# Kernel tuning notes

Hardware: AMD Instinct MI355X
Metric: run time of the kernel (lower is better)

Reference implementation:

```python
import jax, jax.numpy as jnp
import numpy as np

B, C, H, W = 32, 1536, 14, 14   # input is (B*4, C, H, W); joint -> (B, C, 2H, 2W)
CI = C // 2                     # non-local inter_channels
EPS = 1e-5


def conv1x1(x, w, b):
    # x: (b, cin, h, w); w: (cout, cin); b: (cout,)
    return jnp.einsum('bchw,oc->bohw', x, w) + b[None, :, None, None]


def maxpool2(x):
    b, c, h, w = x.shape
    return x.reshape(b, c, h // 2, 2, w // 2, 2).max(axis=(3, 5))


def setup_inputs():
    key = jax.random.key(0)
    ks = jax.random.split(key, 12)
    s = 0.02
    return {
        'x': jax.random.normal(ks[0], (B * 4, C, H, W), jnp.float32),
        'w_theta': jax.random.normal(ks[1], (CI, C), jnp.float32) * s,
        'b_theta': jnp.zeros((CI,), jnp.float32),
        'w_phi': jax.random.normal(ks[2], (CI, C), jnp.float32) * s,
        'b_phi': jnp.zeros((CI,), jnp.float32),
        'w_g': jax.random.normal(ks[3], (CI, C), jnp.float32) * s,
        'b_g': jnp.zeros((CI,), jnp.float32),
        'w_W': jax.random.normal(ks[4], (C, CI), jnp.float32) * s,
        'b_W': jnp.zeros((C,), jnp.float32),
        'bn_gamma': jax.random.normal(ks[5], (C,), jnp.float32) * 0.1 + 1.0,
        'bn_beta': jax.random.normal(ks[6], (C,), jnp.float32) * 0.1,
        'bn_mean': jax.random.normal(ks[7], (C,), jnp.float32) * 0.1,
        'bn_var': jnp.ones((C,), jnp.float32),
    }


def joint(x):
    # (B*4, C, H, W) -> (B, C, 2H, 2W): 4 views tiled in a 2x2 grid
    x4 = x.reshape(B, 4, C, H, W)
    top = jnp.concatenate([x4[:, 0], x4[:, 1]], axis=-1)   # (B, C, H, 2W)
    bot = jnp.concatenate([x4[:, 2], x4[:, 3]], axis=-1)
    return jnp.concatenate([top, bot], axis=-2)             # (B, C, 2H, 2W)


def reference(x, w_theta, b_theta, w_phi, b_phi, w_g, b_g, w_W, b_W,
              bn_gamma, bn_beta, bn_mean, bn_var):
    xj = joint(x)                                           # (B, C, Hj, Wj)
    b, c, hj, wj = xj.shape
    n = hj * wj                                             # 784 query positions

    theta = conv1x1(xj, w_theta, b_theta).reshape(b, CI, n)             # (B, CI, N)
    phi = maxpool2(conv1x1(xj, w_phi, b_phi)).reshape(b, CI, -1)        # (B, CI, N/4)
    g = maxpool2(conv1x1(xj, w_g, b_g)).reshape(b, CI, -1)              # (B, CI, N/4)

    f = jnp.einsum('bcn,bcm->bnm', theta, phi)              # (B, N, N/4)
    attn = jax.nn.softmax(f, axis=-1)
    y = jnp.einsum('bnm,bcm->bcn', attn, g)                 # (B, CI, N)
    y = y.reshape(b, CI, hj, wj)

    w_y = conv1x1(y, w_W, b_W)
    # BatchNorm (inference form)
    inv = jax.lax.rsqrt(bn_var + EPS)
    w_y = (w_y - bn_mean[None, :, None, None]) * (bn_gamma * inv)[None, :, None, None] \
          + bn_beta[None, :, None, None]
    return w_y + xj
```

## Files before the change

### kernel.cpp

```cpp
#include <hip/hip_runtime.h>
#include <hip/hip_bf16.h>

typedef __attribute__((ext_vector_type(8))) _Float16 f16x8;
typedef __attribute__((ext_vector_type(4))) float f32x4;
typedef __attribute__((ext_vector_type(4))) unsigned short us4;
typedef __attribute__((ext_vector_type(8))) unsigned short us8;

#define B_   32
#define C_   1536
#define CI_  768
#define N_   784
#define S_   196
#define MP_  224
#define MK_  196

__device__ __forceinline__ unsigned short f2h(float f) {
    _Float16 h = (_Float16)f;
    return __builtin_bit_cast(unsigned short, h);
}
__device__ __forceinline__ f32x4 mfma_f16(f16x8 a, f16x8 b, f32x4 c) {
    return __builtin_amdgcn_mfma_f32_16x16x32_f16(a, b, c, 0, 0, 0);
}
__device__ __forceinline__ void gl_lds16(const unsigned short* g, unsigned short* l) {
    __builtin_amdgcn_global_load_lds(
        (const __attribute__((address_space(1))) unsigned int*)g,
        (__attribute__((address_space(3))) unsigned int*)l, 16, 0, 0);
}

__device__ __forceinline__ void stage23(const unsigned short* Arow,
                                        const unsigned short* Brow,
                                        unsigned short* A_s, unsigned short* B_s,
                                        int k0, int stride,
                                        int wv, int l4r, int l4c_sw) {
    for (int c = wv; c < 23; c += 4) {
        if (c < 16) {
            gl_lds16(Arow + (size_t)(c * 16 + l4r) * stride + k0 + l4c_sw * 8,
                     A_s + c * 512);
        } else {
            int cb = c - 16;
            gl_lds16(Brow + (size_t)(cb * 16 + l4r) * stride + k0 + l4c_sw * 8,
                     B_s + cb * 512);
        }
    }
}

__device__ __forceinline__ void stage24(const unsigned short* Arow,
                                        const unsigned short* Brow,
                                        unsigned short* A_s, unsigned short* B_s,
                                        int k0, int stride,
                                        int wv, int l4r, int l4c_sw) {
    for (int c = wv; c < 24; c += 4) {
        if (c < 16) {
            gl_lds16(Arow + (size_t)(c * 16 + l4r) * stride + k0 + l4c_sw * 8,
                     A_s + c * 512);
        } else {
            int cb = c - 16;
            gl_lds16(Brow + (size_t)(cb * 16 + l4r) * stride + k0 + l4c_sw * 8,
                     B_s + cb * 512);
        }
    }
}

#define PIPE_WAIT_BARRIER()                                   \
    do {                                                      \
        asm volatile("s_waitcnt vmcnt(6)" ::: "memory");      \
        __builtin_amdgcn_s_barrier();                         \
        __builtin_amdgcn_sched_barrier(0);                    \
    } while (0)

__global__ __launch_bounds__(256) void k_cvt(const float* __restrict__ src,
                                             unsigned short* __restrict__ dst,
                                             int count4) {
    int idx = blockIdx.x * 256 + threadIdx.x;
    if (idx < count4) {
        f32x4 v = ((const f32x4*)src)[idx];
        us4 o;
        o[0] = f2h(v[0]); o[1] = f2h(v[1]); o[2] = f2h(v[2]); o[3] = f2h(v[3]);
        ((us4*)dst)[idx] = o;
    }
}

__global__ __launch_bounds__(256) void k_build_xjT(const float* __restrict__ x,
                                                   unsigned short* __restrict__ xjT) {
    __shared__ __align__(16) unsigned short lds[196 * 40];
    int c0 = blockIdx.x * 32;
    int b4 = blockIdx.y;
    int b = b4 >> 2, v = b4 & 3;
    int tid = threadIdx.x;
    const float* src = x + ((size_t)b4 * C_ + c0) * S_;
    for (int idx = tid; idx < 32 * 49; idx += 256) {
        int cl = idx / 49;
        int sq = idx - cl * 49;
        f32x4 val = *(const f32x4*)(src + (size_t)cl * S_ + sq * 4);
        int s = sq * 4;
        lds[(s + 0) * 40 + cl] = f2h(val[0]);
        lds[(s + 1) * 40 + cl] = f2h(val[1]);
        lds[(s + 2) * 40 + cl] = f2h(val[2]);
        lds[(s + 3) * 40 + cl] = f2h(val[3]);
    }
    __syncthreads();
    int rowbase = (v >> 1) * 14, colbase = (v & 1) * 14;
    for (int idx = tid; idx < 196 * 4; idx += 256) {
        int s = idx >> 2, ch = idx & 3;
        int hh = s / 14, ww = s - hh * 14;
        int n = (rowbase + hh) * 28 + colbase + ww;
        us8 val = *(const us8*)(&lds[s * 40 + ch * 8]);
        *(us8*)(xjT + ((size_t)b * N_ + n) * C_ + c0 + ch * 8) = val;
    }
}

__global__ __launch_bounds__(256) void k_bnprep(const float* __restrict__ bw,
                                                const float* __restrict__ gamma,
                                                const float* __restrict__ beta,
                                                const float* __restrict__ mean,
                                                const float* __restrict__ var,
                                                float* __restrict__ scale,
                                                float* __restrict__ shift) {
    int i = blockIdx.x * 256 + threadIdx.x;
    if (i < C_) {
        float sc = gamma[i] * rsqrtf(var[i] + 1e-5f);
        scale[i] = sc;
        shift[i] = (bw[i] - mean[i]) * sc + beta[i];
    }
}

#define COMPUTE_STEP4(As, Bs)                                                     \
    {                                                                             \
        f16x8 a0_ = *(const f16x8*)(&(As)[((wv * 4 + 0) * 16 + lr) * 32 + rcol]); \
        f16x8 a1_ = *(const f16x8*)(&(As)[((wv * 4 + 1) * 16 + lr) * 32 + rcol]); \
        f16x8 a2_ = *(const f16x8*)(&(As)[((wv * 4 + 2) * 16 + lr) * 32 + rcol]); \
        f16x8 a3_ = *(const f16x8*)(&(As)[((wv * 4 + 3) * 16 + lr) * 32 + rcol]); \
        _Pragma("unroll")                                                         \
        for (int j = 0; j < 7; ++j) {                                             \
            f16x8 bb = *(const f16x8*)(&(Bs)[(j * 16 + lr) * 32 + rcol]);         \
            acc[0][j] = mfma_f16(a0_, bb, acc[0][j]);                             \
            acc[1][j] = mfma_f16(a1_, bb, acc[1][j]);                             \
            acc[2][j] = mfma_f16(a2_, bb, acc[2][j]);                             \
            acc[3][j] = mfma_f16(a3_, bb, acc[3][j]);                             \
        }                                                                         \
    }

#define COMPUTE_STEP4P(As, Bs)                                                    \
    {                                                                             \
        __builtin_amdgcn_s_setprio(1);                                            \
        COMPUTE_STEP4(As, Bs);                                                    \
        __builtin_amdgcn_s_setprio(0);                                            \
    }

__global__ __launch_bounds__(256, 3) void k_conv3(
    const unsigned short* __restrict__ xjT,
    const unsigned short* __restrict__ wf,
    const float* __restrict__ b_theta, const float* __restrict__ b_phi,
    const float* __restrict__ b_g,
    unsigned short* __restrict__ theta_T, unsigned short* __restrict__ phi_p,
    unsigned short* __restrict__ g_p) {
    __shared__ __align__(16) unsigned char smem[47104];
    unsigned short* A0 = (unsigned short*)smem;
    unsigned short* B0 = A0 + 8192;
    unsigned short* A1 = A0 + 11776;
    unsigned short* B1 = A0 + 19968;
    float* fLDS = (float*)smem;

    int f = blockIdx.x;
    int xcd = f & 7, g = f >> 3;
    int pg = g / 9, tm = g - pg * 9;
    int pair = xcd * 28 + pg;
    int tn = pair % 7, b = pair / 7;

    int o0 = tm * 256, n0 = tn * 112;
    int region = o0 / 768;
    int obase = o0 - region * 768;
    const float* bias = (region == 0) ? b_theta : (region == 1) ? b_phi : b_g;

    int tid = threadIdx.x;
    int wv = tid >> 6, lane = tid & 63, lr = lane & 15, quad = lane >> 4;
    int l4r = lane >> 2, l4c = lane & 3;
    int l4c_sw = l4c ^ ((l4r >> 1) & 3);
    int rcol = (quad ^ ((lr >> 1) & 3)) * 8;

    f32x4 acc[4][7];
#pragma unroll
    for (int i = 0; i < 4; ++i)
#pragma unroll
        for (int j = 0; j < 7; ++j) acc[i][j] = (f32x4){0.f, 0.f, 0.f, 0.f};

    const unsigned short* Arow = wf + (size_t)o0 * C_;
    const unsigned short* Brow = xjT + ((size_t)b * N_ + n0) * C_;

    stage23(Arow, Brow, A0, B0, 0, C_, wv, l4r, l4c_sw);
    __syncthreads();
    for (int kk = 0; kk < 48; kk += 2) {
        stage23(Arow, Brow, A1, B1, (kk + 1) * 32, C_, wv, l4r, l4c_sw);
        COMPUTE_STEP4(A0, B0);
        __syncthreads();
        if (kk + 2 < 48)
            stage23(Arow, Brow, A0, B0, (kk + 2) * 32, C_, wv, l4r, l4c_sw);
        COMPUTE_STEP4(A1, B1);
        __syncthreads();
    }

    for (int h = 0; h < 4; ++h) {
        if (wv == h) {
#pragma unroll
            for (int i = 0; i < 4; ++i)
#pragma unroll
                for (int j = 0; j < 7; ++j)
#pragma unroll
                    for (int r = 0; r < 4; ++r) {
                        int o_rel = i * 16 + quad * 4 + r;
                        int n_l = j * 16 + lr;
                        fLDS[o_rel * 112 + n_l] = acc[i][j][r];
                    }
        }
        __syncthreads();
        if (region == 0) {
            for (int idx = tid; idx < 112 * 8; idx += 256) {
                int n_l = idx >> 3, ch = idx & 7;
                us8 outv;
#pragma unroll
                for (int k = 0; k < 8; ++k) {
                    int o_rel = ch * 8 + k;
                    float val = fLDS[o_rel * 112 + n_l] + bias[obase + h * 64 + o_rel];
                    outv[k] = f2h(val);
                }
                *(us8*)(theta_T + ((size_t)b * N_ + n0 + n_l) * CI_ + o0 + h * 64 + ch * 8) = outv;
            }
        } else if (region == 1) {
            for (int idx = tid; idx < 28 * 8; idx += 256) {
                int mm = idx >> 3, ch = idx & 7;
                int a = mm / 14, mw = mm - a * 14;
                int m = (tn * 2 + a) * 14 + mw;
                int sb = a * 56 + mw * 2;
                us8 outv;
#pragma unroll
                for (int k = 0; k < 8; ++k) {
                    int o_rel = ch * 8 + k;
                    const float* p = &fLDS[o_rel * 112 + sb];
                    float val = fmaxf(fmaxf(p[0], p[1]), fmaxf(p[28], p[29]));
                    val += bias[obase + h * 64 + o_rel];
                    outv[k] = f2h(val);
                }
                *(us8*)(phi_p + ((size_t)b * MP_ + m) * CI_ + obase + h * 64 + ch * 8) = outv;
            }
        } else {
            for (int idx = tid; idx < 128; idx += 256) {
                int o_rel = idx >> 1, a = idx & 1;
                int ci = obase + h * 64 + o_rel;
                unsigned short* dst = g_p + ((size_t)b * CI_ + ci) * MP_ + (tn * 2 + a) * 14;
                const float* p0 = &fLDS[o_rel * 112 + a * 56];
                float bv = bias[obase + h * 64 + o_rel];
#pragma unroll
                for (int mw = 0; mw < 14; ++mw) {
                    const float* p = p0 + mw * 2;
                    dst[mw] = f2h(fmaxf(fmaxf(p[0], p[1]), fmaxf(p[28], p[29])) + bv);
                }
            }
        }
        __syncthreads();
    }
}

__global__ __launch_bounds__(256) void k_attn(
    const unsigned short* __restrict__ theta_T,
    const unsigned short* __restrict__ phi_p,
    const unsigned short* __restrict__ g_p,
    unsigned short* __restrict__ y) {
    __shared__ __align__(16) float f_s[32 * 228];

    int f = blockIdx.x;
    int xcd = f & 7, g = f >> 3;
    int idx2 = xcd * 100 + g;
    int b = idx2 / 25, nb = idx2 - b * 25;
    int n0 = nb * 32;
    int tid = threadIdx.x, wv = tid >> 6, lane = tid & 63, lr = lane & 15, quad = lane >> 4;
    int mf0 = wv * 4;
    int nm = (mf0 + 4 <= 14) ? 4 : (14 - mf0);

    int na0 = n0 + lr;       if (na0 > 783) na0 = 783;
    int na1 = n0 + 16 + lr;  if (na1 > 783) na1 = 783;
    const unsigned short* tA0 = theta_T + ((size_t)b * N_ + na0) * CI_ + quad * 8;
    const unsigned short* tA1 = theta_T + ((size_t)b * N_ + na1) * CI_ + quad * 8;

    f32x4 acc[2][4];
#pragma unroll
    for (int i = 0; i < 2; ++i)
#pragma unroll
        for (int j = 0; j < 4; ++j) acc[i][j] = (f32x4){0.f, 0.f, 0.f, 0.f};

    for (int kk = 0; kk < 24; ++kk) {
        int k0 = kk * 32;
        f16x8 a0 = *(const f16x8*)(tA0 + k0);
        f16x8 a1 = *(const f16x8*)(tA1 + k0);
        for (int j = 0; j < nm; ++j) {
            f16x8 bb = *(const f16x8*)(phi_p +
                ((size_t)b * MP_ + (mf0 + j) * 16 + lr) * CI_ + k0 + quad * 8);
            acc[0][j] = mfma_f16(a0, bb, acc[0][j]);
            acc[1][j] = mfma_f16(a1, bb, acc[1][j]);
        }
    }
    for (int i = 0; i < 2; ++i)
        for (int j = 0; j < nm; ++j)
#pragma unroll
            for (int r = 0; r < 4; ++r)
                f_s[(i * 16 + quad * 4 + r) * 228 + (mf0 + j) * 16 + lr] = acc[i][j][r];
    __syncthreads();
    {
        int row = tid >> 3, sub = tid & 7;
        float* rowp = f_s + row * 228;
        int m0 = sub * 28;
        float mx = -1e30f;
#pragma unroll
        for (int m = 0; m < 28; ++m)
            if (m0 + m < MK_) mx = fmaxf(mx, rowp[m0 + m]);
        mx = fmaxf(mx, __shfl_xor(mx, 1));
        mx = fmaxf(mx, __shfl_xor(mx, 2));
        mx = fmaxf(mx, __shfl_xor(mx, 4));
        float sum = 0.f;
#pragma unroll
        for (int m = 0; m < 28; ++m) {
            float e = (m0 + m < MK_) ? __expf(rowp[m0 + m] - mx) : 0.f;
            rowp[m0 + m] = e;
            sum += e;
        }
        sum += __shfl_xor(sum, 1);
        sum += __shfl_xor(sum, 2);
        sum += __shfl_xor(sum, 4);
        float inv = 1.0f / sum;
#pragma unroll
        for (int m = 0; m < 28; ++m) rowp[m0 + m] *= inv;
    }
    __syncthreads();
    for (int c3 = 0; c3 < 3; ++c3) {
        int ci0 = c3 * 256;
        f32x4 acc2[2][4];
#pragma unroll
        for (int i = 0; i < 2; ++i)
#pragma unroll
            for (int j = 0; j < 4; ++j) acc2[i][j] = (f32x4){0.f, 0.f, 0.f, 0.f};
        for (int km = 0; km < 7; ++km) {
            int k0 = km * 32;
            f16x8 a[2];
#pragma unroll
            for (int i = 0; i < 2; ++i) {
                const float* fp = &f_s[(i * 16 + lr) * 228 + k0 + quad * 8];
                f16x8 t;
#pragma unroll
                for (int j = 0; j < 8; ++j) t[j] = (_Float16)fp[j];
                a[i] = t;
            }
#pragma unroll
            for (int j = 0; j < 4; ++j) {
                f16x8 bb = *(const f16x8*)(g_p +
                    ((size_t)b * CI_ + ci0 + (wv * 4 + j) * 16 + lr) * MP_ + k0 + quad * 8);
                acc2[0][j] = mfma_f16(a[0], bb, acc2[0][j]);
                acc2[1][j] = mfma_f16(a[1], bb, acc2[1][j]);
            }
        }
#pragma unroll
        for (int i = 0; i < 2; ++i)
#pragma unroll
            for (int j = 0; j < 4; ++j)
#pragma unroll
                for (int r = 0; r < 4; ++r) {
                    int n = n0 + i * 16 + quad * 4 + r;
                    if (n < N_) {
                        int ci = ci0 + (wv * 4 + j) * 16 + lr;
                        y[((size_t)b * N_ + n) * CI_ + ci] = f2h(acc2[i][j][r]);
                    }
                }
    }
}

__global__ __launch_bounds__(256, 2) void k_final(
    const unsigned short* __restrict__ yb,
    const unsigned short* __restrict__ wfW,
    const float* __restrict__ scale, const float* __restrict__ shift,
    const float* __restrict__ x,
    float* __restrict__ out) {
    __shared__ __align__(16) unsigned short smem_us[36864];
    unsigned short* A0 = smem_us;
    unsigned short* B0 = smem_us + 8192;
    unsigned short* A1 = smem_us + 12288;
    unsigned short* B1 = smem_us + 20480;
    unsigned short* A2 = smem_us + 24576;
    unsigned short* B2 = smem_us + 32768;

    int f = blockIdx.x;
    int xcd = f & 7, g = f >> 3;
    int pg = g / 6, tm = g - pg * 6;
    int pair = xcd * 28 + pg;
    int tn = pair % 7, b = pair / 7;

    int o0 = tm * 256, n0 = tn * 112;
    int tid = threadIdx.x, wv = tid >> 6, lane = tid & 63, lr = lane & 15, quad = lane >> 4;
    int l4r = lane >> 2, l4c = lane & 3;
    int l4c_sw = l4c ^ ((l4r >> 1) & 3);
    int rcol = (quad ^ ((lr >> 1) & 3)) * 8;

    f32x4 acc[4][7];
#pragma unroll
    for (int i = 0; i < 4; ++i)
#pragma unroll
        for (int j = 0; j < 7; ++j) acc[i][j] = (f32x4){0.f, 0.f, 0.f, 0.f};

    const unsigned short* Arow = wfW + (size_t)o0 * CI_;
    const unsigned short* Brow = yb + ((size_t)b * N_ + n0) * CI_;

    stage24(Arow, Brow, A0, B0, 0, CI_, wv, l4r, l4c_sw);
    stage24(Arow, Brow, A1, B1, 32, CI_, wv, l4r, l4c_sw);
    for (int kk = 0; kk < 24; kk += 3) {
        PIPE_WAIT_BARRIER();
        stage24(Arow, Brow, A2, B2, (kk + 2 < 24 ? kk + 2 : 23) * 32, CI_, wv, l4r, l4c_sw);
        COMPUTE_STEP4P(A0, B0);
        PIPE_WAIT_BARRIER();
        stage24(Arow, Brow, A0, B0, (kk + 3 < 24 ? kk + 3 : 23) * 32, CI_, wv, l4r, l4c_sw);
        COMPUTE_STEP4P(A1, B1);
        PIPE_WAIT_BARRIER();
        stage24(Arow, Brow, A1, B1, (kk + 4 < 24 ? kk + 4 : 23) * 32, CI_, wv, l4r, l4c_sw);
        COMPUTE_STEP4P(A2, B2);
    }
    asm volatile("s_waitcnt vmcnt(0)" ::: "memory");
    __syncthreads();
#pragma unroll
    for (int i = 0; i < 4; ++i)
#pragma unroll
        for (int r = 0; r < 4; ++r) {
            int o = o0 + (wv * 4 + i) * 16 + quad * 4 + r;
            float sc = scale[o], sh = shift[o];
#pragma unroll
            for (int j = 0; j < 7; ++j) {
                int n = n0 + j * 16 + lr;
                int hh = n / 28, ww = n - hh * 28;
                int vv = ((hh >= 14) ? 2 : 0) + ((ww >= 14) ? 1 : 0);
                int s = (hh - ((hh >= 14) ? 14 : 0)) * 14 + (ww - ((ww >= 14) ? 14 : 0));
                float xval = x[((size_t)(b * 4 + vv) * C_ + o) * S_ + s];
                out[((size_t)b * C_ + o) * N_ + n] = acc[i][j][r] * sc + sh + xval;
            }
        }
}

extern "C" void kernel_launch(void* const* d_in, const int* in_sizes, int n_in,
                              void* d_out, int out_size, void* d_ws, size_t ws_size,
                              hipStream_t stream) {
    (void)in_sizes; (void)n_in; (void)out_size; (void)ws_size;
    const float* x       = (const float*)d_in[0];
    const float* w_theta = (const float*)d_in[1];
    const float* b_theta = (const float*)d_in[2];
    const float* w_phi   = (const float*)d_in[3];
    const float* b_phi   = (const float*)d_in[4];
    const float* w_g     = (const float*)d_in[5];
    const float* b_g     = (const float*)d_in[6];
    const float* w_W     = (const float*)d_in[7];
    const float* b_W     = (const float*)d_in[8];
    const float* gamma   = (const float*)d_in[9];
    const float* beta    = (const float*)d_in[10];
    const float* mean    = (const float*)d_in[11];
    const float* var     = (const float*)d_in[12];

    char* ob = (char*)d_out;
    unsigned short* xjT     = (unsigned short*)(ob);
    unsigned short* theta_T = (unsigned short*)(ob + 77070336);
    unsigned short* phi_p   = (unsigned short*)(ob + 115605504);
    unsigned short* g_p     = (unsigned short*)(ob + 126615552);
    unsigned short* wf3     = (unsigned short*)(ob + 137625600);

    char* ws = (char*)d_ws;
    unsigned short* yb    = (unsigned short*)(ws);
    unsigned short* wfW   = (unsigned short*)(ws + 38535168);
    float*          scale = (float*)(ws + 40894464);
    float*          shift = (float*)(ws + 40900608);

    hipMemsetAsync(phi_p, 0, 11010048, stream);
    hipMemsetAsync(g_p, 0, 11010048, stream);

    k_bnprep<<<6, 256, 0, stream>>>(b_W, gamma, beta, mean, var, scale, shift);
    k_cvt<<<1152, 256, 0, stream>>>(w_theta, wf3,                294912);
    k_cvt<<<1152, 256, 0, stream>>>(w_phi,   wf3 + 768 * 1536,   294912);
    k_cvt<<<1152, 256, 0, stream>>>(w_g,     wf3 + 2 * 768 * 1536, 294912);
    k_cvt<<<1152, 256, 0, stream>>>(w_W,     wfW,                294912);
    k_build_xjT<<<dim3(48, 128), 256, 0, stream>>>(x, xjT);
    k_conv3<<<2016, 256, 0, stream>>>(xjT, wf3, b_theta, b_phi, b_g,
                                      theta_T, phi_p, g_p);
    k_attn<<<800, 256, 0, stream>>>(theta_T, phi_p, g_p, yb);
    k_final<<<1344, 256, 0, stream>>>(yb, wfW, scale, shift, x,
                                      (float*)d_out);
}
```

Baseline: 756.8 us.

## Load conv weight A-fragments directly to registers, stage only B in LDS

In the fused theta/phi/g 1x1 conv kernel, each wave now loads its private 64-row weight fragments straight from global memory into registers, prefetching one k-step ahead. Only the activation tile goes through LDS with double buffering. This shrinks LDS use and removes the A LDS round trip, but it adds uncoalesced global loads per lane. It also drops the occupancy hint of 3 from launch_bounds, which may raise register pressure or lower occupancy. The loop changes from two k-steps per iteration to one, with a barrier on every step.

```diff
diff --git a/kernel.cpp b/kernel.cpp
--- a/kernel.cpp
+++ b/kernel.cpp
@@ -27,20 +27,12 @@
         (__attribute__((address_space(3))) unsigned int*)l, 16, 0, 0);
 }
 
-__device__ __forceinline__ void stage23(const unsigned short* Arow,
-                                        const unsigned short* Brow,
-                                        unsigned short* A_s, unsigned short* B_s,
-                                        int k0, int stride,
+__device__ __forceinline__ void stageB7(const unsigned short* Brow,
+                                        unsigned short* B_s, int k0,
                                         int wv, int l4r, int l4c_sw) {
-    for (int c = wv; c < 23; c += 4) {
-        if (c < 16) {
-            gl_lds16(Arow + (size_t)(c * 16 + l4r) * stride + k0 + l4c_sw * 8,
-                     A_s + c * 512);
-        } else {
-            int cb = c - 16;
-            gl_lds16(Brow + (size_t)(cb * 16 + l4r) * stride + k0 + l4c_sw * 8,
-                     B_s + cb * 512);
-        }
+    for (int c = wv; c < 7; c += 4) {
+        gl_lds16(Brow + (size_t)(c * 16 + l4r) * C_ + k0 + l4c_sw * 8,
+                 B_s + c * 512);
     }
 }
 
@@ -147,18 +139,30 @@
         __builtin_amdgcn_s_setprio(0);                                            \
     }
 
-__global__ __launch_bounds__(256, 3) void k_conv3(
+#define COMPUTE_REGA(Bs)                                                          \
+    {                                                                             \
+        __builtin_amdgcn_s_setprio(1);                                            \
+        _Pragma("unroll")                                                         \
+        for (int j = 0; j < 7; ++j) {                                             \
+            f16x8 bb = *(const f16x8*)(&(Bs)[(j * 16 + lr) * 32 + rcol]);         \
+            acc[0][j] = mfma_f16(aC0, bb, acc[0][j]);                             \
+            acc[1][j] = mfma_f16(aC1, bb, acc[1][j]);                             \
+            acc[2][j] = mfma_f16(aC2, bb, acc[2][j]);                             \
+            acc[3][j] = mfma_f16(aC3, bb, acc[3][j]);                             \
+        }                                                                         \
+        __builtin_amdgcn_s_setprio(0);                                            \
+    }
+
+__global__ __launch_bounds__(256) void k_conv3(
     const unsigned short* __restrict__ xjT,
     const unsigned short* __restrict__ wf,
     const float* __restrict__ b_theta, const float* __restrict__ b_phi,
     const float* __restrict__ b_g,
     unsigned short* __restrict__ theta_T, unsigned short* __restrict__ phi_p,
     unsigned short* __restrict__ g_p) {
-    __shared__ __align__(16) unsigned char smem[47104];
-    unsigned short* A0 = (unsigned short*)smem;
-    unsigned short* B0 = A0 + 8192;
-    unsigned short* A1 = A0 + 11776;
-    unsigned short* B1 = A0 + 19968;
+    __shared__ __align__(16) unsigned char smem[28672];
+    unsigned short* B0 = (unsigned short*)smem;
+    unsigned short* B1 = B0 + 3584;
     float* fLDS = (float*)smem;
 
     int f = blockIdx.x;
@@ -184,19 +188,27 @@
 #pragma unroll
         for (int j = 0; j < 7; ++j) acc[i][j] = (f32x4){0.f, 0.f, 0.f, 0.f};
 
-    const unsigned short* Arow = wf + (size_t)o0 * C_;
     const unsigned short* Brow = xjT + ((size_t)b * N_ + n0) * C_;
-
-    stage23(Arow, Brow, A0, B0, 0, C_, wv, l4r, l4c_sw);
+    const unsigned short* Awq = wf + (size_t)(o0 + wv * 64 + lr) * C_ + quad * 8;
+
+    f16x8 aC0 = *(const f16x8*)(Awq + 0 * 16 * C_);
+    f16x8 aC1 = *(const f16x8*)(Awq + 1 * 16 * C_);
+    f16x8 aC2 = *(const f16x8*)(Awq + 2 * 16 * C_);
+    f16x8 aC3 = *(const f16x8*)(Awq + 3 * 16 * C_);
+    stageB7(Brow, B0, 0, wv, l4r, l4c_sw);
     __syncthreads();
-    for (int kk = 0; kk < 48; kk += 2) {
-        stage23(Arow, Brow, A1, B1, (kk + 1) * 32, C_, wv, l4r, l4c_sw);
-        COMPUTE_STEP4(A0, B0);
+    for (int kk = 0; kk < 48; ++kk) {
+        unsigned short* Bc = (kk & 1) ? B1 : B0;
+        unsigned short* Bn = (kk & 1) ? B0 : B1;
+        int k1 = (kk + 1 < 48) ? (kk + 1) * 32 : 47 * 32;
+        if (kk + 1 < 48) stageB7(Brow, Bn, k1, wv, l4r, l4c_sw);
+        f16x8 aN0 = *(const f16x8*)(Awq + k1 + 0 * 16 * C_);
+        f16x8 aN1 = *(const f16x8*)(Awq + k1 + 1 * 16 * C_);
+        f16x8 aN2 = *(const f16x8*)(Awq + k1 + 2 * 16 * C_);
+        f16x8 aN3 = *(const f16x8*)(Awq + k1 + 3 * 16 * C_);
+        COMPUTE_REGA(Bc);
         __syncthreads();
-        if (kk + 2 < 48)
-            stage23(Arow, Brow, A0, B0, (kk + 2) * 32, C_, wv, l4r, l4c_sw);
-        COMPUTE_STEP4(A1, B1);
-        __syncthreads();
+        aC0 = aN0; aC1 = aN1; aC2 = aN2; aC3 = aN3;
     }
 
     for (int h = 0; h < 4; ++h) {
```

New measurement: 782.6 us. 3.4% more time.

## Rework conv3 pipeline with vmcnt-based waits and store softmax probs as fp16

Applied to the files above, without the earlier changes.

The conv3 GEMM loop drops full __syncthreads and instead issues a barrier before staging, then waits only on older loads with a partial vmcnt wait. It also uses 24-chunk staging (with a clamped redundant last load) and prioritised compute steps. The attention kernel now keeps softmax rows in registers and writes normalised probabilities as fp16 into LDS, so the second GEMM reads f16x8 vectors directly instead of converting fp32 elements each time. The aim is more overlap between global-to-LDS loads and MFMA work and less LDS traffic and conversion. The costs are slightly more LDS per block and extra redundant loads on the final iterations.

```diff
diff --git a/kernel.cpp b/kernel.cpp
--- a/kernel.cpp
+++ b/kernel.cpp
@@ -25,23 +25,6 @@
     __builtin_amdgcn_global_load_lds(
         (const __attribute__((address_space(1))) unsigned int*)g,
         (__attribute__((address_space(3))) unsigned int*)l, 16, 0, 0);
-}
-
-__device__ __forceinline__ void stage23(const unsigned short* Arow,
-                                        const unsigned short* Brow,
-                                        unsigned short* A_s, unsigned short* B_s,
-                                        int k0, int stride,
-                                        int wv, int l4r, int l4c_sw) {
-    for (int c = wv; c < 23; c += 4) {
-        if (c < 16) {
-            gl_lds16(Arow + (size_t)(c * 16 + l4r) * stride + k0 + l4c_sw * 8,
-                     A_s + c * 512);
-        } else {
-            int cb = c - 16;
-            gl_lds16(Brow + (size_t)(cb * 16 + l4r) * stride + k0 + l4c_sw * 8,
-                     B_s + cb * 512);
-        }
-    }
 }
 
 __device__ __forceinline__ void stage24(const unsigned short* Arow,
@@ -61,11 +44,11 @@
     }
 }
 
-#define PIPE_WAIT_BARRIER()                                   \
+#define WAIT6_BARRIER()                                       \
     do {                                                      \
         asm volatile("s_waitcnt vmcnt(6)" ::: "memory");      \
+        __builtin_amdgcn_sched_barrier(0);                    \
         __builtin_amdgcn_s_barrier();                         \
-        __builtin_amdgcn_sched_barrier(0);                    \
     } while (0)
 
 __global__ __launch_bounds__(256) void k_cvt(const float* __restrict__ src,
@@ -154,11 +137,11 @@
     const float* __restrict__ b_g,
     unsigned short* __restrict__ theta_T, unsigned short* __restrict__ phi_p,
     unsigned short* __restrict__ g_p) {
-    __shared__ __align__(16) unsigned char smem[47104];
+    __shared__ __align__(16) unsigned char smem[49152];
     unsigned short* A0 = (unsigned short*)smem;
     unsigned short* B0 = A0 + 8192;
-    unsigned short* A1 = A0 + 11776;
-    unsigned short* B1 = A0 + 19968;
+    unsigned short* A1 = A0 + 12288;
+    unsigned short* B1 = A0 + 20480;
     float* fLDS = (float*)smem;
 
     int f = blockIdx.x;
@@ -187,17 +170,19 @@
     const unsigned short* Arow = wf + (size_t)o0 * C_;
     const unsigned short* Brow = xjT + ((size_t)b * N_ + n0) * C_;
 
-    stage23(Arow, Brow, A0, B0, 0, C_, wv, l4r, l4c_sw);
+    stage24(Arow, Brow, A0, B0, 0, C_, wv, l4r, l4c_sw);
+    for (int kk = 0; kk < 48; kk += 2) {
+        __builtin_amdgcn_s_barrier();
+        stage24(Arow, Brow, A1, B1, (kk + 1 < 48 ? kk + 1 : 47) * 32, C_, wv, l4r, l4c_sw);
+        WAIT6_BARRIER();
+        COMPUTE_STEP4P(A0, B0);
+        __builtin_amdgcn_s_barrier();
+        stage24(Arow, Brow, A0, B0, (kk + 2 < 48 ? kk + 2 : 47) * 32, C_, wv, l4r, l4c_sw);
+        WAIT6_BARRIER();
+        COMPUTE_STEP4P(A1, B1);
+    }
+    asm volatile("s_waitcnt vmcnt(0)" ::: "memory");
     __syncthreads();
-    for (int kk = 0; kk < 48; kk += 2) {
-        stage23(Arow, Brow, A1, B1, (kk + 1) * 32, C_, wv, l4r, l4c_sw);
-        COMPUTE_STEP4(A0, B0);
-        __syncthreads();
-        if (kk + 2 < 48)
-            stage23(Arow, Brow, A0, B0, (kk + 2) * 32, C_, wv, l4r, l4c_sw);
-        COMPUTE_STEP4(A1, B1);
-        __syncthreads();
-    }
 
     for (int h = 0; h < 4; ++h) {
         if (wv == h) {
@@ -306,30 +291,41 @@
     __syncthreads();
     {
         int row = tid >> 3, sub = tid & 7;
-        float* rowp = f_s + row * 228;
+        const float* rowp = f_s + row * 228;
         int m0 = sub * 28;
+        float v[28];
+#pragma unroll
+        for (int m = 0; m < 28; ++m) v[m] = rowp[m0 + m];
+        __syncthreads();
         float mx = -1e30f;
 #pragma unroll
         for (int m = 0; m < 28; ++m)
-            if (m0 + m < MK_) mx = fmaxf(mx, rowp[m0 + m]);
+            if (m0 + m < MK_) mx = fmaxf(mx, v[m]);
         mx = fmaxf(mx, __shfl_xor(mx, 1));
         mx = fmaxf(mx, __shfl_xor(mx, 2));
         mx = fmaxf(mx, __shfl_xor(mx, 4));
         float sum = 0.f;
 #pragma unroll
         for (int m = 0; m < 28; ++m) {
-            float e = (m0 + m < MK_) ? __expf(rowp[m0 + m] - mx) : 0.f;
-            rowp[m0 + m] = e;
+            float e = (m0 + m < MK_) ? __expf(v[m] - mx) : 0.f;
+            v[m] = e;
             sum += e;
         }
         sum += __shfl_xor(sum, 1);
         sum += __shfl_xor(sum, 2);
         sum += __shfl_xor(sum, 4);
         float inv = 1.0f / sum;
-#pragma unroll
-        for (int m = 0; m < 28; ++m) rowp[m0 + m] *= inv;
+        unsigned short* P16 = (unsigned short*)f_s;
+#pragma unroll
+        for (int q = 0; q < 7; ++q) {
+            us4 ov;
+#pragma unroll
+            for (int r = 0; r < 4; ++r) ov[r] = f2h(v[q * 4 + r] * inv);
+            *(us4*)(P16 + row * 232 + m0 + q * 4) = ov;
+        }
     }
     __syncthreads();
+    const unsigned short* P16 = (const unsigned short*)f_s;
     for (int c3 = 0; c3 < 3; ++c3) {
         int ci0 = c3 * 256;
         f32x4 acc2[2][4];
@@ -339,21 +335,14 @@
             for (int j = 0; j < 4; ++j) acc2[i][j] = (f32x4){0.f, 0.f, 0.f, 0.f};
         for (int km = 0; km < 7; ++km) {
             int k0 = km * 32;
-            f16x8 a[2];
-#pragma unroll
-            for (int i = 0; i < 2; ++i) {
-                const float* fp = &f_s[(i * 16 + lr) * 228 + k0 + quad * 8];
-                f16x8 t;
-#pragma unroll
-                for (int j = 0; j < 8; ++j) t[j] = (_Float16)fp[j];
-                a[i] = t;
-            }
+            f16x8 a0 = *(const f16x8*)(P16 + (0 * 16 + lr) * 232 + k0 + quad * 8);
+            f16x8 a1 = *(const f16x8*)(P16 + (1 * 16 + lr) * 232 + k0 + quad * 8);
 #pragma unroll
             for (int j = 0; j < 4; ++j) {
                 f16x8 bb = *(const f16x8*)(g_p +
                     ((size_t)b * CI_ + ci0 + (wv * 4 + j) * 16 + lr) * MP_ + k0 + quad * 8);
-                acc2[0][j] = mfma_f16(a[0], bb, acc2[0][j]);
-                acc2[1][j] = mfma_f16(a[1], bb, acc2[1][j]);
+                acc2[0][j] = mfma_f16(a0, bb, acc2[0][j]);
+                acc2[1][j] = mfma_f16(a1, bb, acc2[1][j]);
             }
         }
 #pragma unroll
@@ -409,13 +398,13 @@
     stage24(Arow, Brow, A0, B0, 0, CI_, wv, l4r, l4c_sw);
     stage24(Arow, Brow, A1, B1, 32, CI_, wv, l4r, l4c_sw);
     for (int kk = 0; kk < 24; kk += 3) {
-        PIPE_WAIT_BARRIER();
+        WAIT6_BARRIER();
         stage24(Arow, Brow, A2, B2, (kk + 2 < 24 ? kk + 2 : 23) * 32, CI_, wv, l4r, l4c_sw);
         COMPUTE_STEP4P(A0, B0);
-        PIPE_WAIT_BARRIER();
+        WAIT6_BARRIER();
         stage24(Arow, Brow, A0, B0, (kk + 3 < 24 ? kk + 3 : 23) * 32, CI_, wv, l4r, l4c_sw);
         COMPUTE_STEP4P(A1, B1);
-        PIPE_WAIT_BARRIER();
+        WAIT6_BARRIER();
         stage24(Arow, Brow, A1, B1, (kk + 4 < 24 ? kk + 4 : 23) * 32, CI_, wv, l4r, l4c_sw);
         COMPUTE_STEP4P(A2, B2);
     }
```

Result: no change. 755.3 us (-0.2%).
